# Kernel tuning notes

Measured on AMD Instinct MI355X. Metric: run time of the kernel, lower is better.

## Reference

```python
import jax, jax.numpy as jnp
import numpy as np

N = 50000      # number of 'oa' nodes
E = 800000     # edges per metapath
IN_DIM = 128
OUT_DIM = 64   # per-head channels (concat=False -> mean over heads)
HEADS = 4
M = 3          # number of metapaths
NEG_SLOPE = 0.2  # PyG GATConv default leaky_relu slope


def setup_inputs() -> dict:
    key = jax.random.key(0)
    ks = jax.random.split(key, 32)
    inp = {"x": jax.random.normal(ks[0], (N, IN_DIM), jnp.float32)}
    for i in range(M):
        inp[f"edge_index_{i}"] = jax.random.randint(ks[1 + i], (2, E), 0, N, jnp.int32)
        inp[f"W_{i}"] = jax.random.normal(ks[4 + i], (IN_DIM, HEADS * OUT_DIM), jnp.float32) * (1.0 / np.sqrt(IN_DIM))
        inp[f"att_src_{i}"] = jax.random.normal(ks[7 + i], (HEADS, OUT_DIM), jnp.float32) * 0.1
        inp[f"att_dst_{i}"] = jax.random.normal(ks[10 + i], (HEADS, OUT_DIM), jnp.float32) * 0.1
        inp[f"bias_{i}"] = jnp.zeros((OUT_DIM,), jnp.float32)
    inp["proj_W"] = jax.random.normal(ks[20], (OUT_DIM, OUT_DIM), jnp.float32) * (1.0 / np.sqrt(OUT_DIM))
    inp["proj_b"] = jnp.zeros((OUT_DIM,), jnp.float32)
    inp["attn_vec"] = jax.random.normal(ks[21], (OUT_DIM,), jnp.float32) * 0.1
    return inp


def _gat_conv(x, edge_index, W, att_src, att_dst, bias):
    """PyG GATConv(in,out,heads,concat=False), eval mode, add_self_loops=True."""
    loop = jnp.arange(N, dtype=edge_index.dtype)
    src = jnp.concatenate([edge_index[0], loop])  # [E+N]
    dst = jnp.concatenate([edge_index[1], loop])
    h = (x @ W).reshape(N, HEADS, OUT_DIM)                 # [N,H,C]
    a_src = jnp.einsum('nhc,hc->nh', h, att_src)           # [N,H]
    a_dst = jnp.einsum('nhc,hc->nh', h, att_dst)
    e = jax.nn.leaky_relu(a_src[src] + a_dst[dst], NEG_SLOPE)  # [E+N,H]
    # edge softmax over incoming edges of each dst node (numerically stable)
    emax = jax.ops.segment_max(e, dst, num_segments=N)
    e = jnp.exp(e - emax[dst])
    denom = jax.ops.segment_sum(e, dst, num_segments=N)
    alpha = e / denom[dst]                                 # [E+N,H]; denom>0 via self loops
    out = jax.ops.segment_sum(h[src] * alpha[:, :, None], dst, num_segments=N)  # [N,H,C]
    return out.mean(axis=1) + bias                         # concat=False -> head mean


def reference(x, edge_index_0, edge_index_1, edge_index_2,
              W_0, W_1, W_2, att_src_0, att_src_1, att_src_2,
              att_dst_0, att_dst_1, att_dst_2, bias_0, bias_1, bias_2,
              proj_W, proj_b, attn_vec):
    eis = (edge_index_0, edge_index_1, edge_index_2)
    Ws = (W_0, W_1, W_2)
    a_s = (att_src_0, att_src_1, att_src_2)
    a_d = (att_dst_0, att_dst_1, att_dst_2)
    bs = (bias_0, bias_1, bias_2)
    z = [jax.nn.elu(_gat_conv(x, eis[i], Ws[i], a_s[i], a_d[i], bs[i])) for i in range(M)]
    z_stack = jnp.stack(z, axis=1)                          # [N,M,C]
    weights = jnp.tanh(z_stack @ proj_W + proj_b)           # [N,M,C]
    scores = jnp.einsum('nmc,c->nm', weights, attn_vec)     # [N,M]
    beta = jax.nn.softmax(scores, axis=1)                   # [N,M]
    z_final = jnp.einsum('nmc,nm->nc', z_stack, beta)       # [N,C]
    return z_final, beta
```

## Files before the change

### kernel.cpp

```cpp
#include <hip/hip_runtime.h>
#include <hip/hip_bf16.h>
#include <math.h>

#define NN 50000
#define EE 800000
#define IND 128
#define OUTD 64
#define NH 4
#define HC 256
#define WSZ 448
#define NWN 112
#define WCAP 8192
#define BATCH 2048
#define NBATCH ((EE + BATCH - 1) / BATCH)
#define NMT 3125
#define CVTB 6250

typedef unsigned short u16;
typedef __attribute__((ext_vector_type(8))) short short8v;
typedef __attribute__((ext_vector_type(4))) float f32x4;
typedef __attribute__((ext_vector_type(2))) _Float16 half2v;

__device__ __forceinline__ float lrelu(float v) { return v > 0.f ? v : 0.2f * v; }
__device__ __forceinline__ u16 f2b(float f) {
  __hip_bfloat16 h = __float2bfloat16(f);
  return __builtin_bit_cast(u16, h);
}
__device__ __forceinline__ float b2f(u16 u) {
  return __uint_as_float((unsigned)u << 16);
}
__device__ __forceinline__ u16 f2h(float f) {
  _Float16 h = (_Float16)f;
  return __builtin_bit_cast(u16, h);
}
__device__ __forceinline__ float h2f(u16 u) {
  return (float)__builtin_bit_cast(_Float16, u);
}
__device__ __forceinline__ unsigned packh2(float a, float b) {
  half2v v = {(_Float16)a, (_Float16)b};
  return __builtin_bit_cast(unsigned, v);
}
__device__ __forceinline__ float dot2h(unsigned hpair, unsigned apair, float acc) {
#if __has_builtin(__builtin_amdgcn_fdot2)
  return __builtin_amdgcn_fdot2(__builtin_bit_cast(half2v, hpair),
                                __builtin_bit_cast(half2v, apair), acc, false);
#else
  acc = fmaf(h2f((u16)(hpair & 0xffff)), h2f((u16)(apair & 0xffff)), acc);
  return fmaf(h2f((u16)(hpair >> 16)), h2f((u16)(apair >> 16)), acc);
#endif
}

__global__ __launch_bounds__(256) void k_part(const int* __restrict__ ei0,
                                              const int* __restrict__ ei1,
                                              const int* __restrict__ ei2,
                                              int* __restrict__ gcur,
                                              unsigned int* __restrict__ glist) {
  __shared__ unsigned int stage[BATCH];
  __shared__ int cnt[NWN], strt[NWN], gbase[NWN];
  const int m = blockIdx.y;
  const int* ei = m == 0 ? ei0 : (m == 1 ? ei1 : ei2);
  const int e0 = blockIdx.x * BATCH;
  const int tid = threadIdx.x;
  if (tid < NWN) cnt[tid] = 0;
  __syncthreads();
  int bk[8], rk[8];
  unsigned int pk[8];
#pragma unroll
  for (int k = 0; k < 8; ++k) {
    const int e = e0 + k * 256 + tid;
    bk[k] = -1;
    rk[k] = 0;
    pk[k] = 0;
    if (e < EE) {
      const int d = ei[EE + e];
      const int s = ei[e];
      const int b = d / WSZ;
      bk[k] = b;
      pk[k] = ((unsigned)d << 16) | (unsigned)s;
      rk[k] = atomicAdd(&cnt[b], 1);
    }
  }
  __syncthreads();
  if (tid < 64) {
    const int base = tid * 2;
    const int c0 = (base + 0 < NWN) ? cnt[base + 0] : 0;
    const int c1 = (base + 1 < NWN) ? cnt[base + 1] : 0;
    const int tot = c0 + c1;
    int run = tot;
#pragma unroll
    for (int off = 1; off < 64; off <<= 1) {
      const int u = __shfl_up(run, off, 64);
      if (tid >= off) run += u;
    }
    int ex = run - tot;
    if (base + 0 < NWN) { strt[base + 0] = ex; ex += c0; }
    if (base + 1 < NWN) { strt[base + 1] = ex; }
  }
  __syncthreads();
  if (tid < NWN && cnt[tid] > 0)
    gbase[tid] = atomicAdd(&gcur[m * NWN + tid], cnt[tid]);
#pragma unroll
  for (int k = 0; k < 8; ++k)
    if (bk[k] >= 0) stage[strt[bk[k]] + rk[k]] = pk[k];
  __syncthreads();
  const int unit = tid >> 3;
  const int l8 = tid & 7;
  for (int b = unit; b < NWN; b += 32) {
    const int len = cnt[b];
    if (len == 0) continue;
    const int st = strt[b];
    const int gb = gbase[b];
    unsigned int* dst = glist + (size_t)(m * NWN + b) * WCAP;
    for (int i = l8; i < len; i += 8)
      if (gb + i < WCAP) dst[gb + i] = stage[st + i];
  }
}

__global__ __launch_bounds__(256) void k_sort(unsigned int* glist,
                                              const int* __restrict__ gcur,
                                              int* __restrict__ rowptr) {
  __shared__ u16 srt[WCAP];
  __shared__ int cnt[WSZ], row[WSZ + 1], cur[WSZ];
  const int m = blockIdx.y;
  const int w = blockIdx.x;
  const int tid = threadIdx.x;
  const int ne = min(gcur[m * NWN + w], WCAP);
  unsigned int* gl = glist + (size_t)(m * NWN + w) * WCAP;
  for (int i = tid; i < WSZ; i += 256) cnt[i] = 0;
  __syncthreads();
  for (int i = tid; i < ne; i += 256)
    atomicAdd(&cnt[(int)(gl[i] >> 16) - w * WSZ], 1);
  __syncthreads();
  if (tid < 64) {
    const int base = tid * 7;
    int c[7], tot = 0;
#pragma unroll
    for (int j = 0; j < 7; ++j) {
      const int idx = base + j;
      c[j] = (idx < WSZ) ? cnt[idx] : 0;
      tot += c[j];
    }
    int run = tot;
#pragma unroll
    for (int off = 1; off < 64; off <<= 1) {
      const int u = __shfl_up(run, off, 64);
      if (tid >= off) run += u;
    }
    int ex = run - tot;
#pragma unroll
    for (int j = 0; j < 7; ++j) {
      const int idx = base + j;
      if (idx < WSZ) { row[idx] = ex; cur[idx] = ex; ex += c[j]; }
    }
    if (tid == 63) row[WSZ] = ne;
  }
  __syncthreads();
  for (int i = tid; i < ne; i += 256) {
    const unsigned int v = gl[i];
    const int dl = (int)(v >> 16) - w * WSZ;
    const int p = atomicAdd(&cur[dl], 1);
    srt[p] = (u16)(v & 0xffffu);
  }
  __syncthreads();
  u16* cdst = (u16*)gl;
  for (int i = tid; i < ne; i += 256) cdst[i] = srt[i];
  int* rp = rowptr + (size_t)(m * NWN + w) * (WSZ + 1);
  for (int i = tid; i <= WSZ; i += 256) rp[i] = row[i];
}

__global__ __launch_bounds__(256) void k_prep(const float* __restrict__ x,
                                              u16* __restrict__ hi,
                                              u16* __restrict__ lo,
                                              const float* __restrict__ W0,
                                              const float* __restrict__ W1,
                                              const float* __restrict__ W2,
                                              const float* __restrict__ as0,
                                              const float* __restrict__ as1,
                                              const float* __restrict__ as2,
                                              const float* __restrict__ ad0,
                                              const float* __restrict__ ad1,
                                              const float* __restrict__ ad2,
                                              u16* __restrict__ wt,
                                              float* __restrict__ attS,
                                              float* __restrict__ attD) {
  const int bx = blockIdx.x;
  if (bx < CVTB) {
    const int i = (bx * 256 + threadIdx.x) * 4;
    const float4 v = *(const float4*)(x + i);
    ushort4 h, l;
    h.x = f2b(v.x); l.x = f2b(v.x - b2f(h.x));
    h.y = f2b(v.y); l.y = f2b(v.y - b2f(h.y));
    h.z = f2b(v.z); l.z = f2b(v.z - b2f(h.z));
    h.w = f2b(v.w); l.w = f2b(v.w - b2f(h.w));
    *(ushort4*)(hi + i) = h;
    *(ushort4*)(lo + i) = l;
    return;
  }
  const int b = bx - CVTB;
  const int m = b >> 4;
  const int kc = b & 15;
  const float* W = m == 0 ? W0 : (m == 1 ? W1 : W2);
  const int col = threadIdx.x;
  const int colp = (col & 63) * 4 + (col >> 6);
#pragma unroll
  for (int kk = 0; kk < 8; ++kk) {
    const int k = kc * 8 + kk;
    wt[(size_t)m * 32768 + colp * IND + k] = f2b(W[k * HC + col]);
  }
  if (kc == 0) {
    const float* as = m == 0 ? as0 : (m == 1 ? as1 : as2);
    const float* ad = m == 0 ? ad0 : (m == 1 ? ad1 : ad2);
    attS[m * HC + colp] = as[col];
    attD[m * HC + colp] = ad[col];
  }
}

__global__ __launch_bounds__(256) void k_mgemm(const u16* __restrict__ xhi,
                                               const u16* __restrict__ xlo,
                                               const u16* __restrict__ wt,
                                               const float* __restrict__ attS,
                                               const float* __restrict__ attD,
                                               u16* __restrict__ H16,
                                               float* __restrict__ a_src,
                                               float* __restrict__ a_dst) {
  const int tid = threadIdx.x;
  const int wid = tid >> 6;
  const int l = tid & 63;
  const int l15 = l & 15;
  const int lq = l >> 4;
  const int mt = blockIdx.x * 4 + wid;
  if (mt >= NMT) return;
  const int m0 = mt * 16;
  const size_t abase = (size_t)(m0 + l15) * IND + lq * 8;
  const u16* pa = xhi + abase;
  const u16* pl = xlo + abase;
  const u16* pb = wt + l15 * IND + lq * 8;
  f32x4 acc[16];
#pragma unroll
  for (int nt = 0; nt < 16; ++nt) acc[nt] = (f32x4){0.f, 0.f, 0.f, 0.f};
#pragma unroll
  for (int ks = 0; ks < 4; ++ks) {
    const short8v ahi = *(const short8v*)(pa + ks * 32);
    const short8v alo = *(const short8v*)(pl + ks * 32);
#pragma unroll
    for (int nt = 0; nt < 16; nt += 2) {
      const short8v b0 = *(const short8v*)(pb + (nt + 0) * 16 * IND + ks * 32);
      const short8v b1 = *(const short8v*)(pb + (nt + 1) * 16 * IND + ks * 32);
      acc[nt]     = __builtin_amdgcn_mfma_f32_16x16x32_bf16(ahi, b0, acc[nt],     0, 0, 0);
      acc[nt + 1] = __builtin_amdgcn_mfma_f32_16x16x32_bf16(ahi, b1, acc[nt + 1], 0, 0, 0);
      acc[nt]     = __builtin_amdgcn_mfma_f32_16x16x32_bf16(alo, b0, acc[nt],     0, 0, 0);
      acc[nt + 1] = __builtin_amdgcn_mfma_f32_16x16x32_bf16(alo, b1, acc[nt + 1], 0, 0, 0);
    }
  }
#pragma unroll
  for (int nt = 0; nt < 16; ++nt) {
#pragma unroll
    for (int r = 0; r < 4; ++r)
      H16[(size_t)(m0 + lq * 4 + r) * HC + nt * 16 + l15] = f2h(acc[nt][r]);
  }
  float asv[16], adv[16];
#pragma unroll
  for (int nt = 0; nt < 16; ++nt) {
    asv[nt] = attS[nt * 16 + l15];
    adv[nt] = attD[nt * 16 + l15];
  }
#pragma unroll
  for (int r = 0; r < 4; ++r) {
    float ps = 0.f, pd = 0.f;
#pragma unroll
    for (int nt = 0; nt < 16; ++nt) {
      ps = fmaf(acc[nt][r], asv[nt], ps);
      pd = fmaf(acc[nt][r], adv[nt], pd);
    }
    ps += __shfl_xor(ps, 4, 64); ps += __shfl_xor(ps, 8, 64);
    pd += __shfl_xor(pd, 4, 64); pd += __shfl_xor(pd, 8, 64);
    if (l15 < 4) {
      const int n = m0 + lq * 4 + r;
      a_src[n * NH + l15] = ps;
      a_dst[n * NH + l15] = pd;
    }
  }
}

__global__ __launch_bounds__(256) void k_aggr(const unsigned int* __restrict__ glist_m,
                                              const int* __restrict__ rowptr,
                                              const u16* __restrict__ H16,
                                              const float* __restrict__ a_src,
                                              const float* __restrict__ a_dst,
                                              const float* __restrict__ bias,
                                              u16* __restrict__ zb) {
  __shared__ uint4 slot[4][64];
  const int wid = threadIdx.x >> 6;
  const int c = threadIdx.x & 63;
  const int d = blockIdx.x * 4 + wid;
  const int w = d / WSZ;
  const int dl = d - w * WSZ;
  const int* rp = rowptr + (size_t)w * (WSZ + 1);
  const int r0 = rp[dl];
  const int nb = min(rp[dl + 1] - r0, 64);
  const u16* cw = (const u16*)(glist_m + (size_t)w * WCAP);
  const float4 adv = *(const float4*)&a_dst[d * NH];
  float4 evr = make_float4(0.f, 0.f, 0.f, 0.f);
  int sj = 0;
  if (c < nb) {
    sj = cw[r0 + c];
    const float4 asv = *(const float4*)&a_src[sj * NH];
    evr.x = __expf(lrelu(asv.x + adv.x));
    evr.y = __expf(lrelu(asv.y + adv.y));
    evr.z = __expf(lrelu(asv.z + adv.z));
    evr.w = __expf(lrelu(asv.w + adv.w));
  }
  float den0 = evr.x, den1 = evr.y, den2 = evr.z, den3 = evr.w;
#pragma unroll
  for (int mk = 32; mk; mk >>= 1) {
    den0 += __shfl_xor(den0, mk, 64);
    den1 += __shfl_xor(den1, mk, 64);
    den2 += __shfl_xor(den2, mk, 64);
    den3 += __shfl_xor(den3, mk, 64);
  }
  const float4 asl = *(const float4*)&a_src[d * NH];
  const float e0s = __expf(lrelu(asl.x + adv.x));
  const float e1s = __expf(lrelu(asl.y + adv.y));
  const float e2s = __expf(lrelu(asl.z + adv.z));
  const float e3s = __expf(lrelu(asl.w + adv.w));
  den0 += e0s; den1 += e1s; den2 += e2s; den3 += e3s;
  const float rd0 = 0.25f * __builtin_amdgcn_rcpf(den0);
  const float rd1 = 0.25f * __builtin_amdgcn_rcpf(den1);
  const float rd2 = 0.25f * __builtin_amdgcn_rcpf(den2);
  const float rd3 = 0.25f * __builtin_amdgcn_rcpf(den3);
  if (c < nb) {
    uint4 sv;
    sv.x = packh2(evr.x * rd0, evr.y * rd1);
    sv.y = packh2(evr.z * rd2, evr.w * rd3);
    sv.z = (unsigned)(sj * (HC * 2));
    sv.w = 0;
    slot[wid][c] = sv;
  }
  const ushort4 hs = *(const ushort4*)&H16[(size_t)d * HC + c * 4];
  float res = e0s * rd0 * h2f(hs.x);
  res = fmaf(e1s * rd1, h2f(hs.y), res);
  res = fmaf(e2s * rd2, h2f(hs.z), res);
  res = fmaf(e3s * rd3, h2f(hs.w), res);
  const unsigned char* Hb = (const unsigned char*)H16;
  const int c8 = c * 8;
  float accA = 0.f, accB = 0.f, accC = 0.f, accD = 0.f;
  int j = 0;
  for (; j + 4 <= nb; j += 4) {
    const uint4 sa = slot[wid][j + 0];
    const uint4 sb = slot[wid][j + 1];
    const uint4 sc = slot[wid][j + 2];
    const uint4 sd = slot[wid][j + 3];
    const uint2 ha = *(const uint2*)(Hb + (size_t)sa.z + c8);
    const uint2 hb = *(const uint2*)(Hb + (size_t)sb.z + c8);
    const uint2 hc = *(const uint2*)(Hb + (size_t)sc.z + c8);
    const uint2 hd = *(const uint2*)(Hb + (size_t)sd.z + c8);
    accA = dot2h(ha.x, sa.x, accA); accA = dot2h(ha.y, sa.y, accA);
    accB = dot2h(hb.x, sb.x, accB); accB = dot2h(hb.y, sb.y, accB);
    accC = dot2h(hc.x, sc.x, accC); accC = dot2h(hc.y, sc.y, accC);
    accD = dot2h(hd.x, sd.x, accD); accD = dot2h(hd.y, sd.y, accD);
  }
  for (; j < nb; ++j) {
    const uint4 sa = slot[wid][j];
    const uint2 ha = *(const uint2*)(Hb + (size_t)sa.z + c8);
    accA = dot2h(ha.x, sa.x, accA);
    accA = dot2h(ha.y, sa.y, accA);
  }
  res += (accA + accB) + (accC + accD);
  res += bias[c];
  res = res > 0.f ? res : __expf(res) - 1.f;
  zb[(size_t)d * OUTD + c] = f2b(res);
}

__global__ __launch_bounds__(256) void k_sem(const u16* __restrict__ zb,
                                             const float* __restrict__ proj_W,
                                             const float* __restrict__ proj_b,
                                             const float* __restrict__ attn_vec,
                                             float* __restrict__ out) {
  __shared__ float pw[64 * 64];
  __shared__ float zl[3][16][OUTD];
  const int tid = threadIdx.x;
  const int n0 = blockIdx.x * 16;
  for (int i = tid; i < 1024; i += 256)
    ((float4*)pw)[i] = ((const float4*)proj_W)[i];
#pragma unroll
  for (int mm = 0; mm < 3; ++mm) {
    const ushort4 v = ((const ushort4*)(zb + ((size_t)mm * NN + n0) * OUTD))[tid];
    float4 f;
    f.x = b2f(v.x); f.y = b2f(v.y); f.z = b2f(v.z); f.w = b2f(v.w);
    *(float4*)&zl[mm][tid >> 4][(tid & 15) * 4] = f;
  }
  __syncthreads();
  const int wid = tid >> 6;
  const int c = tid & 63;
  const float pb = proj_b[c];
  const float av = attn_vec[c];
  for (int nl = 0; nl < 4; ++nl) {
    const int node = wid * 4 + nl;
    float s[3];
#pragma unroll
    for (int mm = 0; mm < 3; ++mm) {
      float a0 = pb, a1 = 0.f, a2 = 0.f, a3 = 0.f;
#pragma unroll
      for (int kk = 0; kk < 16; ++kk) {
        a0 = fmaf(zl[mm][node][kk],      pw[kk * 64 + c],        a0);
        a1 = fmaf(zl[mm][node][16 + kk], pw[(16 + kk) * 64 + c], a1);
        a2 = fmaf(zl[mm][node][32 + kk], pw[(32 + kk) * 64 + c], a2);
        a3 = fmaf(zl[mm][node][48 + kk], pw[(48 + kk) * 64 + c], a3);
      }
      float xx = (a0 + a1) + (a2 + a3);
      xx = fminf(xx, 40.f);
      const float t = __expf(2.f * xx);
      const float th = (t - 1.f) * __builtin_amdgcn_rcpf(t + 1.f);
      float p = th * av;
#pragma unroll
      for (int mk = 32; mk; mk >>= 1) p += __shfl_xor(p, mk, 64);
      s[mm] = p;
    }
    const float mx = fmaxf(s[0], fmaxf(s[1], s[2]));
    const float e0 = __expf(s[0] - mx), e1 = __expf(s[1] - mx), e2 = __expf(s[2] - mx);
    const float inv = 1.0f / (e0 + e1 + e2);
    const float b0 = e0 * inv, b1 = e1 * inv, b2 = e2 * inv;
    const int n = n0 + node;
    const float zf = zl[0][node][c] * b0 + zl[1][node][c] * b1 + zl[2][node][c] * b2;
    out[(size_t)n * OUTD + c] = zf;
    if (c < 3) out[(size_t)NN * OUTD + n * 3 + c] = (c == 0 ? b0 : (c == 1 ? b1 : b2));
  }
}

extern "C" void kernel_launch(void* const* d_in, const int* in_sizes, int n_in,
                              void* d_out, int out_size, void* d_ws, size_t ws_size,
                              hipStream_t stream) {
  const float* x = (const float*)d_in[0];
  const int* ei[3];
  const float* W[3];
  const float* as[3];
  const float* ad[3];
  const float* bs[3];

  if (in_sizes[2] != 2 * EE) {
    for (int m = 0; m < 3; ++m) {
      ei[m] = (const int*)d_in[1 + 5 * m];
      W[m]  = (const float*)d_in[2 + 5 * m];
      as[m] = (const float*)d_in[3 + 5 * m];
      ad[m] = (const float*)d_in[4 + 5 * m];
      bs[m] = (const float*)d_in[5 + 5 * m];
    }
  } else {
    for (int m = 0; m < 3; ++m) {
      ei[m] = (const int*)d_in[1 + m];
      W[m]  = (const float*)d_in[4 + m];
      as[m] = (const float*)d_in[7 + m];
      ad[m] = (const float*)d_in[10 + m];
      bs[m] = (const float*)d_in[13 + m];
    }
  }
  const float* proj_W = (const float*)d_in[16];
  const float* proj_b = (const float*)d_in[17];
  const float* attn_vec = (const float*)d_in[18];

  char* ws = (char*)d_ws;
  size_t off = 0;
  u16* x16hi = (u16*)(ws + off);                     off += (size_t)NN * IND * 2;
  u16* x16lo = (u16*)(ws + off);                     off += (size_t)NN * IND * 2;
  u16* H16 = (u16*)(ws + off);                       off += (size_t)NN * HC * 2;
  u16* zb = (u16*)(ws + off);                        off += (size_t)3 * NN * OUTD * 2;
  float* a_srcb = (float*)(ws + off);                off += (size_t)NN * NH * 4;
  float* a_dstb = (float*)(ws + off);                off += (size_t)NN * NH * 4;
  int* gcur = (int*)(ws + off);                      off += (size_t)3 * NWN * 4;
  unsigned int* glist = (unsigned int*)(ws + off);   off += (size_t)3 * NWN * WCAP * 4;
  int* rowptr = (int*)(ws + off);                    off += (size_t)3 * NWN * (WSZ + 1) * 4;
  u16* wt16 = (u16*)(ws + off);                      off += (size_t)3 * HC * IND * 2;
  float* attSp = (float*)(ws + off);                 off += (size_t)3 * HC * 4;
  float* attDp = (float*)(ws + off);                 off += (size_t)3 * HC * 4;

  float* outp = (float*)d_out;

  hipMemsetAsync(gcur, 0, (size_t)3 * NWN * sizeof(int), stream);
  k_part<<<dim3(NBATCH, 3), 256, 0, stream>>>(ei[0], ei[1], ei[2], gcur, glist);
  k_sort<<<dim3(NWN, 3), 256, 0, stream>>>(glist, gcur, rowptr);
  k_prep<<<CVTB + 48, 256, 0, stream>>>(x, x16hi, x16lo,
                                        W[0], W[1], W[2], as[0], as[1], as[2],
                                        ad[0], ad[1], ad[2], wt16, attSp, attDp);

  for (int m = 0; m < 3; ++m) {
    k_mgemm<<<(NMT + 3) / 4, 256, 0, stream>>>(x16hi, x16lo, wt16 + (size_t)m * HC * IND,
                                               attSp + m * HC, attDp + m * HC,
                                               H16, a_srcb, a_dstb);
    k_aggr<<<NN / 4, 256, 0, stream>>>(glist + (size_t)m * NWN * WCAP,
                                       rowptr + (size_t)m * NWN * (WSZ + 1),
                                       H16, a_srcb, a_dstb, bs[m],
                                       zb + (size_t)m * NN * OUTD);
  }
  k_sem<<<NN / 16, 256, 0, stream>>>(zb, proj_W, proj_b, attn_vec, outp);
}
```

Measured before the change: 386.7 us.

## Merge partition and prep kernels, halve windows, batch GEMM/aggregation across metapaths

Folds the edge-partition kernel and the x/W conversion kernel into one launch, so the two independent front-end jobs can share the GPU. Halves the destination window size, doubling the number of windows and k_sort blocks, with smaller per-window capacity. When the workspace is large enough, it runs the feature GEMM and the aggregation for all three metapaths as single launches with a grid y dimension, instead of six sequential launches. The batched path needs separate H/a buffers per metapath, which triples that workspace. If the workspace is too small it falls back to the per-metapath loop.

Result: faster. 343.0 us (-11.3%).

```diff
diff --git a/kernel.cpp b/kernel.cpp
--- a/kernel.cpp
+++ b/kernel.cpp
@@ -8,13 +8,15 @@
 #define OUTD 64
 #define NH 4
 #define HC 256
-#define WSZ 448
-#define NWN 112
-#define WCAP 8192
+#define WSZ 224
+#define NWN 224
+#define WCAP 4096
 #define BATCH 2048
 #define NBATCH ((EE + BATCH - 1) / BATCH)
+#define PB (3 * NBATCH)
 #define NMT 3125
 #define CVTB 6250
+#define WPB 48
 
 typedef unsigned short u16;
 typedef __attribute__((ext_vector_type(8))) short short8v;
@@ -50,69 +52,121 @@
 #endif
 }
 
-__global__ __launch_bounds__(256) void k_part(const int* __restrict__ ei0,
-                                              const int* __restrict__ ei1,
-                                              const int* __restrict__ ei2,
-                                              int* __restrict__ gcur,
-                                              unsigned int* __restrict__ glist) {
+__global__ __launch_bounds__(256) void k_front(const int* __restrict__ ei0,
+                                               const int* __restrict__ ei1,
+                                               const int* __restrict__ ei2,
+                                               int* __restrict__ gcur,
+                                               unsigned int* __restrict__ glist,
+                                               const float* __restrict__ x,
+                                               u16* __restrict__ hi,
+                                               u16* __restrict__ lo,
+                                               const float* __restrict__ W0,
+                                               const float* __restrict__ W1,
+                                               const float* __restrict__ W2,
+                                               const float* __restrict__ as0,
+                                               const float* __restrict__ as1,
+                                               const float* __restrict__ as2,
+                                               const float* __restrict__ ad0,
+                                               const float* __restrict__ ad1,
+                                               const float* __restrict__ ad2,
+                                               u16* __restrict__ wt,
+                                               float* __restrict__ attS,
+                                               float* __restrict__ attD) {
   __shared__ unsigned int stage[BATCH];
   __shared__ int cnt[NWN], strt[NWN], gbase[NWN];
-  const int m = blockIdx.y;
-  const int* ei = m == 0 ? ei0 : (m == 1 ? ei1 : ei2);
-  const int e0 = blockIdx.x * BATCH;
+  const int bx = blockIdx.x;
   const int tid = threadIdx.x;
-  if (tid < NWN) cnt[tid] = 0;
-  __syncthreads();
-  int bk[8], rk[8];
-  unsigned int pk[8];
-#pragma unroll
-  for (int k = 0; k < 8; ++k) {
-    const int e = e0 + k * 256 + tid;
-    bk[k] = -1;
-    rk[k] = 0;
-    pk[k] = 0;
-    if (e < EE) {
-      const int d = ei[EE + e];
-      const int s = ei[e];
-      const int b = d / WSZ;
-      bk[k] = b;
-      pk[k] = ((unsigned)d << 16) | (unsigned)s;
-      rk[k] = atomicAdd(&cnt[b], 1);
-    }
-  }
-  __syncthreads();
-  if (tid < 64) {
-    const int base = tid * 2;
-    const int c0 = (base + 0 < NWN) ? cnt[base + 0] : 0;
-    const int c1 = (base + 1 < NWN) ? cnt[base + 1] : 0;
-    const int tot = c0 + c1;
-    int run = tot;
-#pragma unroll
-    for (int off = 1; off < 64; off <<= 1) {
-      const int u = __shfl_up(run, off, 64);
-      if (tid >= off) run += u;
-    }
-    int ex = run - tot;
-    if (base + 0 < NWN) { strt[base + 0] = ex; ex += c0; }
-    if (base + 1 < NWN) { strt[base + 1] = ex; }
-  }
-  __syncthreads();
-  if (tid < NWN && cnt[tid] > 0)
-    gbase[tid] = atomicAdd(&gcur[m * NWN + tid], cnt[tid]);
-#pragma unroll
-  for (int k = 0; k < 8; ++k)
-    if (bk[k] >= 0) stage[strt[bk[k]] + rk[k]] = pk[k];
-  __syncthreads();
-  const int unit = tid >> 3;
-  const int l8 = tid & 7;
-  for (int b = unit; b < NWN; b += 32) {
-    const int len = cnt[b];
-    if (len == 0) continue;
-    const int st = strt[b];
-    const int gb = gbase[b];
-    unsigned int* dst = glist + (size_t)(m * NWN + b) * WCAP;
-    for (int i = l8; i < len; i += 8)
-      if (gb + i < WCAP) dst[gb + i] = stage[st + i];
+  if (bx < PB) {
+    const int m = bx / NBATCH;
+    const int e0 = (bx - m * NBATCH) * BATCH;
+    const int* ei = m == 0 ? ei0 : (m == 1 ? ei1 : ei2);
+    if (tid < NWN) cnt[tid] = 0;
+    __syncthreads();
+    int bk[8], rk[8];
+    unsigned int pk[8];
+#pragma unroll
+    for (int k = 0; k < 8; ++k) {
+      const int e = e0 + k * 256 + tid;
+      bk[k] = -1; rk[k] = 0; pk[k] = 0;
+      if (e < EE) {
+        const int d = ei[EE + e];
+        const int s = ei[e];
+        const int b = d / WSZ;
+        bk[k] = b;
+        pk[k] = ((unsigned)d << 16) | (unsigned)s;
+        rk[k] = atomicAdd(&cnt[b], 1);
+      }
+    }
+    __syncthreads();
+    if (tid < 64) {
+      const int base = tid * 4;
+      int c0 = 0, c1 = 0, c2 = 0, c3 = 0;
+      if (base + 0 < NWN) c0 = cnt[base + 0];
+      if (base + 1 < NWN) c1 = cnt[base + 1];
+      if (base + 2 < NWN) c2 = cnt[base + 2];
+      if (base + 3 < NWN) c3 = cnt[base + 3];
+      const int tot = c0 + c1 + c2 + c3;
+      int run = tot;
+#pragma unroll
+      for (int off = 1; off < 64; off <<= 1) {
+        const int u = __shfl_up(run, off, 64);
+        if (tid >= off) run += u;
+      }
+      int ex = run - tot;
+      if (base + 0 < NWN) { strt[base + 0] = ex; ex += c0; }
+      if (base + 1 < NWN) { strt[base + 1] = ex; ex += c1; }
+      if (base + 2 < NWN) { strt[base + 2] = ex; ex += c2; }
+      if (base + 3 < NWN) { strt[base + 3] = ex; }
+    }
+    __syncthreads();
+    if (tid < NWN && cnt[tid] > 0)
+      gbase[tid] = atomicAdd(&gcur[m * NWN + tid], cnt[tid]);
+#pragma unroll
+    for (int k = 0; k < 8; ++k)
+      if (bk[k] >= 0) stage[strt[bk[k]] + rk[k]] = pk[k];
+    __syncthreads();
+    const int unit = tid >> 3;
+    const int l8 = tid & 7;
+    for (int b = unit; b < NWN; b += 32) {
+      const int len = cnt[b];
+      if (len == 0) continue;
+      const int st = strt[b];
+      const int gb = gbase[b];
+      unsigned int* dst = glist + (size_t)(m * NWN + b) * WCAP;
+      for (int i = l8; i < len; i += 8)
+        if (gb + i < WCAP) dst[gb + i] = stage[st + i];
+    }
+    return;
+  }
+  const int px = bx - PB;
+  if (px < CVTB) {
+    const int i = (px * 256 + tid) * 4;
+    const float4 v = *(const float4*)(x + i);
+    ushort4 h, l;
+    h.x = f2b(v.x); l.x = f2b(v.x - b2f(h.x));
+    h.y = f2b(v.y); l.y = f2b(v.y - b2f(h.y));
+    h.z = f2b(v.z); l.z = f2b(v.z - b2f(h.z));
+    h.w = f2b(v.w); l.w = f2b(v.w - b2f(h.w));
+    *(ushort4*)(hi + i) = h;
+    *(ushort4*)(lo + i) = l;
+    return;
+  }
+  const int b = px - CVTB;
+  const int m = b >> 4;
+  const int kc = b & 15;
+  const float* W = m == 0 ? W0 : (m == 1 ? W1 : W2);
+  const int col = tid;
+  const int colp = (col & 63) * 4 + (col >> 6);
+#pragma unroll
+  for (int kk = 0; kk < 8; ++kk) {
+    const int k = kc * 8 + kk;
+    wt[(size_t)m * (HC * IND) + colp * IND + k] = f2b(W[k * HC + col]);
+  }
+  if (kc == 0) {
+    const float* as = m == 0 ? as0 : (m == 1 ? as1 : as2);
+    const float* ad = m == 0 ? ad0 : (m == 1 ? ad1 : ad2);
+    attS[m * HC + colp] = as[col];
+    attD[m * HC + colp] = ad[col];
   }
 }
 
@@ -126,20 +180,19 @@
   const int tid = threadIdx.x;
   const int ne = min(gcur[m * NWN + w], WCAP);
   unsigned int* gl = glist + (size_t)(m * NWN + w) * WCAP;
-  for (int i = tid; i < WSZ; i += 256) cnt[i] = 0;
+  if (tid < WSZ) cnt[tid] = 0;
   __syncthreads();
   for (int i = tid; i < ne; i += 256)
     atomicAdd(&cnt[(int)(gl[i] >> 16) - w * WSZ], 1);
   __syncthreads();
   if (tid < 64) {
-    const int base = tid * 7;
-    int c[7], tot = 0;
-#pragma unroll
-    for (int j = 0; j < 7; ++j) {
-      const int idx = base + j;
-      c[j] = (idx < WSZ) ? cnt[idx] : 0;
-      tot += c[j];
-    }
+    const int base = tid * 4;
+    int c0 = 0, c1 = 0, c2 = 0, c3 = 0;
+    if (base + 0 < WSZ) c0 = cnt[base + 0];
+    if (base + 1 < WSZ) c1 = cnt[base + 1];
+    if (base + 2 < WSZ) c2 = cnt[base + 2];
+    if (base + 3 < WSZ) c3 = cnt[base + 3];
+    const int tot = c0 + c1 + c2 + c3;
     int run = tot;
 #pragma unroll
     for (int off = 1; off < 64; off <<= 1) {
@@ -147,11 +200,10 @@
       if (tid >= off) run += u;
     }
     int ex = run - tot;
-#pragma unroll
-    for (int j = 0; j < 7; ++j) {
-      const int idx = base + j;
-      if (idx < WSZ) { row[idx] = ex; cur[idx] = ex; ex += c[j]; }
-    }
+    if (base + 0 < WSZ) { row[base + 0] = ex; cur[base + 0] = ex; ex += c0; }
+    if (base + 1 < WSZ) { row[base + 1] = ex; cur[base + 1] = ex; ex += c1; }
+    if (base + 2 < WSZ) { row[base + 2] = ex; cur[base + 2] = ex; ex += c2; }
+    if (base + 3 < WSZ) { row[base + 3] = ex; cur[base + 3] = ex; }
     if (tid == 63) row[WSZ] = ne;
   }
   __syncthreads();
@@ -165,64 +217,25 @@
   u16* cdst = (u16*)gl;
   for (int i = tid; i < ne; i += 256) cdst[i] = srt[i];
   int* rp = rowptr + (size_t)(m * NWN + w) * (WSZ + 1);
-  for (int i = tid; i <= WSZ; i += 256) rp[i] = row[i];
-}
-
-__global__ __launch_bounds__(256) void k_prep(const float* __restrict__ x,
-                                              u16* __restrict__ hi,
-                                              u16* __restrict__ lo,
-                                              const float* __restrict__ W0,
-                                              const float* __restrict__ W1,
-                                              const float* __restrict__ W2,
-                                              const float* __restrict__ as0,
-                                              const float* __restrict__ as1,
-                                              const float* __restrict__ as2,
-                                              const float* __restrict__ ad0,
-                                              const float* __restrict__ ad1,
-                                              const float* __restrict__ ad2,
-                                              u16* __restrict__ wt,
-                                              float* __restrict__ attS,
-                                              float* __restrict__ attD) {
-  const int bx = blockIdx.x;
-  if (bx < CVTB) {
-    const int i = (bx * 256 + threadIdx.x) * 4;
-    const float4 v = *(const float4*)(x + i);
-    ushort4 h, l;
-    h.x = f2b(v.x); l.x = f2b(v.x - b2f(h.x));
-    h.y = f2b(v.y); l.y = f2b(v.y - b2f(h.y));
-    h.z = f2b(v.z); l.z = f2b(v.z - b2f(h.z));
-    h.w = f2b(v.w); l.w = f2b(v.w - b2f(h.w));
-    *(ushort4*)(hi + i) = h;
-    *(ushort4*)(lo + i) = l;
-    return;
-  }
-  const int b = bx - CVTB;
-  const int m = b >> 4;
-  const int kc = b & 15;
-  const float* W = m == 0 ? W0 : (m == 1 ? W1 : W2);
-  const int col = threadIdx.x;
-  const int colp = (col & 63) * 4 + (col >> 6);
-#pragma unroll
-  for (int kk = 0; kk < 8; ++kk) {
-    const int k = kc * 8 + kk;
-    wt[(size_t)m * 32768 + colp * IND + k] = f2b(W[k * HC + col]);
-  }
-  if (kc == 0) {
-    const float* as = m == 0 ? as0 : (m == 1 ? as1 : as2);
-    const float* ad = m == 0 ? ad0 : (m == 1 ? ad1 : ad2);
-    attS[m * HC + colp] = as[col];
-    attD[m * HC + colp] = ad[col];
-  }
+  if (tid <= WSZ) rp[tid] = row[tid];
 }
 
 __global__ __launch_bounds__(256) void k_mgemm(const u16* __restrict__ xhi,
                                                const u16* __restrict__ xlo,
-                                               const u16* __restrict__ wt,
-                                               const float* __restrict__ attS,
-                                               const float* __restrict__ attD,
-                                               u16* __restrict__ H16,
-                                               float* __restrict__ a_src,
-                                               float* __restrict__ a_dst) {
+                                               const u16* __restrict__ wtB,
+                                               const float* __restrict__ attSB,
+                                               const float* __restrict__ attDB,
+                                               u16* __restrict__ H16B,
+                                               float* __restrict__ a_srcB,
+                                               float* __restrict__ a_dstB,
+                                               int strideH, int strideA) {
+  const int m = blockIdx.y;
+  const u16* wt = wtB + (size_t)m * (HC * IND);
+  const float* attS = attSB + m * HC;
+  const float* attD = attDB + m * HC;
+  u16* H16 = H16B + (size_t)m * strideH;
+  float* a_src = a_srcB + (size_t)m * strideA;
+  float* a_dst = a_dstB + (size_t)m * strideA;
   const int tid = threadIdx.x;
   const int wid = tid >> 6;
   const int l = tid & 63;
@@ -282,20 +295,31 @@
   }
 }
 
-__global__ __launch_bounds__(256) void k_aggr(const unsigned int* __restrict__ glist_m,
-                                              const int* __restrict__ rowptr,
-                                              const u16* __restrict__ H16,
-                                              const float* __restrict__ a_src,
-                                              const float* __restrict__ a_dst,
-                                              const float* __restrict__ bias,
-                                              u16* __restrict__ zb) {
+__global__ __launch_bounds__(256) void k_aggr(const unsigned int* __restrict__ glistB,
+                                              const int* __restrict__ rowptrB,
+                                              const u16* __restrict__ H16B,
+                                              const float* __restrict__ a_srcB,
+                                              const float* __restrict__ a_dstB,
+                                              const float* __restrict__ b0_,
+                                              const float* __restrict__ b1_,
+                                              const float* __restrict__ b2_,
+                                              u16* __restrict__ zbB,
+                                              int strideH, int strideA) {
   __shared__ uint4 slot[4][64];
+  const int m = blockIdx.y;
+  const unsigned int* glist_m = glistB + (size_t)m * NWN * WCAP;
+  const int* rowptrm = rowptrB + (size_t)m * NWN * (WSZ + 1);
+  const u16* H16 = H16B + (size_t)m * strideH;
+  const float* a_src = a_srcB + (size_t)m * strideA;
+  const float* a_dst = a_dstB + (size_t)m * strideA;
+  const float* bias = m == 0 ? b0_ : (m == 1 ? b1_ : b2_);
+  u16* zb = zbB + (size_t)m * NN * OUTD;
   const int wid = threadIdx.x >> 6;
   const int c = threadIdx.x & 63;
   const int d = blockIdx.x * 4 + wid;
   const int w = d / WSZ;
   const int dl = d - w * WSZ;
-  const int* rp = rowptr + (size_t)w * (WSZ + 1);
+  const int* rp = rowptrm + (size_t)w * (WSZ + 1);
   const int r0 = rp[dl];
   const int nb = min(rp[dl + 1] - r0, 64);
   const u16* cw = (const u16*)(glist_m + (size_t)w * WCAP);
@@ -458,14 +482,17 @@
   const float* proj_b = (const float*)d_in[17];
   const float* attn_vec = (const float*)d_in[18];
 
+  const bool batched = (ws_size >= (size_t)139000000);
+  const int nrep = batched ? 3 : 1;
+
   char* ws = (char*)d_ws;
   size_t off = 0;
   u16* x16hi = (u16*)(ws + off);                     off += (size_t)NN * IND * 2;
   u16* x16lo = (u16*)(ws + off);                     off += (size_t)NN * IND * 2;
-  u16* H16 = (u16*)(ws + off);                       off += (size_t)NN * HC * 2;
+  u16* H16 = (u16*)(ws + off);                       off += (size_t)nrep * NN * HC * 2;
   u16* zb = (u16*)(ws + off);                        off += (size_t)3 * NN * OUTD * 2;
-  float* a_srcb = (float*)(ws + off);                off += (size_t)NN * NH * 4;
-  float* a_dstb = (float*)(ws + off);                off += (size_t)NN * NH * 4;
+  float* a_srcb = (float*)(ws + off);                off += (size_t)nrep * NN * NH * 4;
+  float* a_dstb = (float*)(ws + off);                off += (size_t)nrep * NN * NH * 4;
   int* gcur = (int*)(ws + off);                      off += (size_t)3 * NWN * 4;
   unsigned int* glist = (unsigned int*)(ws + off);   off += (size_t)3 * NWN * WCAP * 4;
   int* rowptr = (int*)(ws + off);                    off += (size_t)3 * NWN * (WSZ + 1) * 4;
@@ -476,20 +503,27 @@
   float* outp = (float*)d_out;
 
   hipMemsetAsync(gcur, 0, (size_t)3 * NWN * sizeof(int), stream);
-  k_part<<<dim3(NBATCH, 3), 256, 0, stream>>>(ei[0], ei[1], ei[2], gcur, glist);
+  k_front<<<PB + CVTB + WPB, 256, 0, stream>>>(ei[0], ei[1], ei[2], gcur, glist,
+                                               x, x16hi, x16lo,
+                                               W[0], W[1], W[2], as[0], as[1], as[2],
+                                               ad[0], ad[1], ad[2], wt16, attSp, attDp);
   k_sort<<<dim3(NWN, 3), 256, 0, stream>>>(glist, gcur, rowptr);
-  k_prep<<<CVTB + 48, 256, 0, stream>>>(x, x16hi, x16lo,
-                                        W[0], W[1], W[2], as[0], as[1], as[2],
-                                        ad[0], ad[1], ad[2], wt16, attSp, attDp);
-
-  for (int m = 0; m < 3; ++m) {
-    k_mgemm<<<(NMT + 3) / 4, 256, 0, stream>>>(x16hi, x16lo, wt16 + (size_t)m * HC * IND,
-                                               attSp + m * HC, attDp + m * HC,
-                                               H16, a_srcb, a_dstb);
-    k_aggr<<<NN / 4, 256, 0, stream>>>(glist + (size_t)m * NWN * WCAP,
-                                       rowptr + (size_t)m * NWN * (WSZ + 1),
-                                       H16, a_srcb, a_dstb, bs[m],
-                                       zb + (size_t)m * NN * OUTD);
+
+  if (batched) {
+    k_mgemm<<<dim3((NMT + 3) / 4, 3), 256, 0, stream>>>(
+        x16hi, x16lo, wt16, attSp, attDp, H16, a_srcb, a_dstb, NN * HC, NN * NH);
+    k_aggr<<<dim3(NN / 4, 3), 256, 0, stream>>>(
+        glist, rowptr, H16, a_srcb, a_dstb, bs[0], bs[1], bs[2], zb, NN * HC, NN * NH);
+  } else {
+    for (int m = 0; m < 3; ++m) {
+      k_mgemm<<<dim3((NMT + 3) / 4, 1), 256, 0, stream>>>(
+          x16hi, x16lo, wt16 + (size_t)m * HC * IND, attSp + m * HC, attDp + m * HC,
+          H16, a_srcb, a_dstb, 0, 0);
+      k_aggr<<<dim3(NN / 4, 1), 256, 0, stream>>>(
+          glist + (size_t)m * NWN * WCAP, rowptr + (size_t)m * NWN * (WSZ + 1),
+          H16, a_srcb, a_dstb, bs[m], bs[m], bs[m],
+          zb + (size_t)m * NN * OUTD, 0, 0);
+    }
   }
   k_sem<<<NN / 16, 256, 0, stream>>>(zb, proj_W, proj_b, attn_vec, outp);
 }
```
